# Optimization experiments

Hardware: AMD Instinct MI355X
Metric: run time of the kernel (lower is better)

## Reference

```python
import jax, jax.numpy as jnp
import numpy as np

EPS = 1e-8
TOPK = 10


def setup_inputs() -> dict:
    key = jax.random.key(0)
    kz, ky = jax.random.split(key)
    B, C, T = 128, 512, 512
    Z = jax.random.normal(kz, (B, C, T), dtype=jnp.float32)
    Y = jax.random.normal(ky, (B, C, T), dtype=jnp.float32)
    return {"Z": Z, "Y": Y}


def reference(Z, Y):
    B = Z.shape[0]
    x = Z.reshape(B, -1)  # [B, D]
    y = Y.reshape(B, -1)  # [B, D]
    # cosine similarity: sim[i, j] = x[i] . y[j] / max(|x[i]| * |y[j]|, eps)
    dots = jnp.einsum("id,jd->ij", x, y)  # [B, B]
    xn = jnp.linalg.norm(x, axis=1)  # [B]
    yn = jnp.linalg.norm(y, axis=1)  # [B]
    sim = dots / jnp.maximum(xn[:, None] * yn[None, :], EPS)
    sim = sim.T  # rows now indexed by Y, cols by Z (as in original)
    diags = jnp.arange(B)
    top1accuracy = jnp.mean((jnp.argmax(sim, axis=1) == diags).astype(jnp.float32))
    _, topk_idx = jax.lax.top_k(sim, TOPK)  # [B, 10]
    top10accuracy = jnp.mean(jnp.any(topk_idx == diags[:, None], axis=1).astype(jnp.float32))
    return (top1accuracy, top10accuracy)
```

## Files before the change

kernel.cpp:

```cpp
#include <hip/hip_runtime.h>
#include <hip/hip_bf16.h>
#include <math.h>


#define DIMD 262144

typedef short  bf16x8  __attribute__((ext_vector_type(8)));
typedef float  floatx4 __attribute__((ext_vector_type(4)));

union FragU { uint4 u; bf16x8 v; };

__global__ __launch_bounds__(256, 3)
void mfma_dot_kernel(const float* __restrict__ Z, const float* __restrict__ Y,
                     float* __restrict__ partials, float* __restrict__ norms,
                     int NT) {
    __shared__ __align__(16) ushort planes[4][128][40];
    __shared__ float nrm[256];

    const int tid = threadIdx.x;
    const int lid = tid & 63;
    const int w   = tid >> 6;

    const int srow = tid >> 3;
    const int q    = tid & 7;

    const int m0 = 64 * (w & 1);
    const int n0 = 64 * (w >> 1);
    const int fr = lid & 15;
    const int fk = (lid >> 4) * 8;

    floatx4 acc[4][4];
#pragma unroll
    for (int a = 0; a < 4; ++a)
#pragma unroll
        for (int b = 0; b < 4; ++b)
            acc[a][b] = (floatx4){0.f, 0.f, 0.f, 0.f};

    nrm[tid] = 0.f;

    const size_t kbase = (size_t)blockIdx.x * ((size_t)NT * 32);
    size_t off[4];
#pragma unroll
    for (int i = 0; i < 4; ++i)
        off[i] = (size_t)(32 * i + srow) * DIMD + kbase + 4 * q;

    float4 zr[4], yr[4];
#pragma unroll
    for (int i = 0; i < 4; ++i) zr[i] = *(const float4*)(Z + off[i]);
#pragma unroll
    for (int i = 0; i < 4; ++i) yr[i] = *(const float4*)(Y + off[i]);

#pragma unroll 1
    for (int t = 0; t < NT; ++t) {
        __syncthreads();

#pragma unroll
        for (int i = 0; i < 4; ++i) {
            const float4 v = zr[i];
            const uint h0 = __float_as_uint(v.x) >> 16, h1 = __float_as_uint(v.y) >> 16;
            const uint h2 = __float_as_uint(v.z) >> 16, h3 = __float_as_uint(v.w) >> 16;
            const uint l0 = __float_as_uint(v.x - __uint_as_float(h0 << 16)) >> 16;
            const uint l1 = __float_as_uint(v.y - __uint_as_float(h1 << 16)) >> 16;
            const uint l2 = __float_as_uint(v.z - __uint_as_float(h2 << 16)) >> 16;
            const uint l3 = __float_as_uint(v.w - __uint_as_float(h3 << 16)) >> 16;
            *(uint2*)&planes[0][32 * i + srow][4 * q] =
                make_uint2(h0 | (h1 << 16), h2 | (h3 << 16));
            *(uint2*)&planes[1][32 * i + srow][4 * q] =
                make_uint2(l0 | (l1 << 16), l2 | (l3 << 16));
            const float s = v.x * v.x + v.y * v.y + v.z * v.z + v.w * v.w;
            atomicAdd(&nrm[32 * i + srow], s);
        }
#pragma unroll
        for (int i = 0; i < 4; ++i) {
            const float4 v = yr[i];
            const uint h0 = __float_as_uint(v.x) >> 16, h1 = __float_as_uint(v.y) >> 16;
            const uint h2 = __float_as_uint(v.z) >> 16, h3 = __float_as_uint(v.w) >> 16;
            const uint l0 = __float_as_uint(v.x - __uint_as_float(h0 << 16)) >> 16;
            const uint l1 = __float_as_uint(v.y - __uint_as_float(h1 << 16)) >> 16;
            const uint l2 = __float_as_uint(v.z - __uint_as_float(h2 << 16)) >> 16;
            const uint l3 = __float_as_uint(v.w - __uint_as_float(h3 << 16)) >> 16;
            *(uint2*)&planes[2][32 * i + srow][4 * q] =
                make_uint2(h0 | (h1 << 16), h2 | (h3 << 16));
            *(uint2*)&planes[3][32 * i + srow][4 * q] =
                make_uint2(l0 | (l1 << 16), l2 | (l3 << 16));
            const float s = v.x * v.x + v.y * v.y + v.z * v.z + v.w * v.w;
            atomicAdd(&nrm[128 + 32 * i + srow], s);
        }

        if (t + 1 < NT) {
            const size_t ko = (size_t)(t + 1) * 32;
#pragma unroll
            for (int i = 0; i < 4; ++i) zr[i] = *(const float4*)(Z + off[i] + ko);
#pragma unroll
            for (int i = 0; i < 4; ++i) yr[i] = *(const float4*)(Y + off[i] + ko);
        }

        __syncthreads();

        FragU bh[4], bl[4];
#pragma unroll
        for (int tn = 0; tn < 4; ++tn) {
            bh[tn].u = *(const uint4*)&planes[2][n0 + 16 * tn + fr][fk];
            bl[tn].u = *(const uint4*)&planes[3][n0 + 16 * tn + fr][fk];
        }
#pragma unroll
        for (int tm = 0; tm < 4; ++tm) {
            FragU ah, al;
            ah.u = *(const uint4*)&planes[0][m0 + 16 * tm + fr][fk];
            al.u = *(const uint4*)&planes[1][m0 + 16 * tm + fr][fk];
#pragma unroll
            for (int tn = 0; tn < 4; ++tn) {
                acc[tm][tn] = __builtin_amdgcn_mfma_f32_16x16x32_bf16(ah.v, bh[tn].v, acc[tm][tn], 0, 0, 0);
                acc[tm][tn] = __builtin_amdgcn_mfma_f32_16x16x32_bf16(ah.v, bl[tn].v, acc[tm][tn], 0, 0, 0);
                acc[tm][tn] = __builtin_amdgcn_mfma_f32_16x16x32_bf16(al.v, bh[tn].v, acc[tm][tn], 0, 0, 0);
            }
        }
    }

    __syncthreads();
    atomicAdd(&norms[tid], nrm[tid]);

    float* P = partials + (size_t)blockIdx.x * 16384;
    const int rq = (lid >> 4) * 4;
#pragma unroll
    for (int tm = 0; tm < 4; ++tm)
#pragma unroll
        for (int tn = 0; tn < 4; ++tn)
#pragma unroll
            for (int r = 0; r < 4; ++r)
                P[(size_t)(m0 + 16 * tm + rq + r) * 128 + (n0 + 16 * tn + fr)] =
                    acc[tm][tn][r];
}

#define BK   16
#define LSTR 132
__global__ __launch_bounds__(256)
void dot_norm_atomic(const float* __restrict__ Z, const float* __restrict__ Y,
                     float* __restrict__ dots, float* __restrict__ norms,
                     int KC) {
    __shared__ float lA[BK][LSTR];
    __shared__ float lB[BK][LSTR];
    const int tid = threadIdx.x;
    const int tx = tid & 15, ty = tid >> 4;
    const int r0 = ty * 8, c0 = tx * 8;
    const int rowm = tid >> 2, kq = tid & 3;
    float acc[8][8];
#pragma unroll
    for (int i = 0; i < 8; ++i)
#pragma unroll
        for (int j = 0; j < 8; ++j) acc[i][j] = 0.f;
    float a2s0 = 0.f, a2s1 = 0.f, b2s0 = 0.f, b2s1 = 0.f;
    const size_t kbase = (size_t)blockIdx.x * KC;
    const size_t offA0 = (size_t)rowm * DIMD + kbase + kq * 4;
    const size_t offA1 = (size_t)(rowm + 64) * DIMD + kbase + kq * 4;
    const int niter = KC / BK;
#pragma unroll 1
    for (int t = 0; t < niter; ++t) {
        const size_t ko = (size_t)t * BK;
        const float4 av0 = *(const float4*)(Z + offA0 + ko);
        const float4 av1 = *(const float4*)(Z + offA1 + ko);
        const float4 bv0 = *(const float4*)(Y + offA0 + ko);
        const float4 bv1 = *(const float4*)(Y + offA1 + ko);
        a2s0 += av0.x*av0.x + av0.y*av0.y + av0.z*av0.z + av0.w*av0.w;
        a2s1 += av1.x*av1.x + av1.y*av1.y + av1.z*av1.z + av1.w*av1.w;
        b2s0 += bv0.x*bv0.x + bv0.y*bv0.y + bv0.z*bv0.z + bv0.w*bv0.w;
        b2s1 += bv1.x*bv1.x + bv1.y*bv1.y + bv1.z*bv1.z + bv1.w*bv1.w;
        __syncthreads();
        const int kk = kq * 4;
        lA[kk+0][rowm]    = av0.x; lA[kk+1][rowm]    = av0.y;
        lA[kk+2][rowm]    = av0.z; lA[kk+3][rowm]    = av0.w;
        lA[kk+0][rowm+64] = av1.x; lA[kk+1][rowm+64] = av1.y;
        lA[kk+2][rowm+64] = av1.z; lA[kk+3][rowm+64] = av1.w;
        lB[kk+0][rowm]    = bv0.x; lB[kk+1][rowm]    = bv0.y;
        lB[kk+2][rowm]    = bv0.z; lB[kk+3][rowm]    = bv0.w;
        lB[kk+0][rowm+64] = bv1.x; lB[kk+1][rowm+64] = bv1.y;
        lB[kk+2][rowm+64] = bv1.z; lB[kk+3][rowm+64] = bv1.w;
        __syncthreads();
#pragma unroll
        for (int k = 0; k < BK; ++k) {
            const float4 a0 = *(const float4*)&lA[k][r0];
            const float4 a1 = *(const float4*)&lA[k][r0 + 4];
            const float4 b0 = *(const float4*)&lB[k][c0];
            const float4 b1 = *(const float4*)&lB[k][c0 + 4];
            const float a[8] = {a0.x,a0.y,a0.z,a0.w,a1.x,a1.y,a1.z,a1.w};
            const float b[8] = {b0.x,b0.y,b0.z,b0.w,b1.x,b1.y,b1.z,b1.w};
#pragma unroll
            for (int i = 0; i < 8; ++i)
#pragma unroll
                for (int j = 0; j < 8; ++j)
                    acc[i][j] = fmaf(a[i], b[j], acc[i][j]);
        }
    }
    __syncthreads();
    float* nrm = &lA[0][0];
    nrm[tid] = 0.f;
    __syncthreads();
    atomicAdd(&nrm[rowm],            a2s0);
    atomicAdd(&nrm[rowm + 64],       a2s1);
    atomicAdd(&nrm[128 + rowm],      b2s0);
    atomicAdd(&nrm[128 + rowm + 64], b2s1);
    __syncthreads();
    atomicAdd(&norms[tid], nrm[tid]);
#pragma unroll
    for (int i = 0; i < 8; ++i)
#pragma unroll
        for (int j = 0; j < 8; ++j)
            atomicAdd(&dots[(size_t)(r0 + i) * 128 + (c0 + j)], acc[i][j]);
}

__global__ __launch_bounds__(256)
void reduce_stage1(const float* __restrict__ partials, float* __restrict__ stage,
                   int per_chunk) {
    const int g = blockIdx.x * 256 + threadIdx.x;
    const int f4 = g & 4095;
    const int chunk = g >> 12;
    const float4* p = (const float4*)partials;
    float4 s = make_float4(0.f, 0.f, 0.f, 0.f);
    const size_t base = (size_t)chunk * per_chunk;
    for (int k = 0; k < per_chunk; ++k) {
        const float4 v = p[(base + k) * 4096 + f4];
        s.x += v.x; s.y += v.y; s.z += v.z; s.w += v.w;
    }
    ((float4*)stage)[(size_t)chunk * 4096 + f4] = s;
}

__global__ __launch_bounds__(128)
void rank_kernel(const float* __restrict__ stage, const float* __restrict__ norms,
                 float* __restrict__ out, int nchunks) {
    __shared__ float sim[128];
    __shared__ int cnt;
    const int a = blockIdx.x;
    const int b = threadIdx.x;
    float s = 0.f;
    for (int c = 0; c < nchunks; ++c)
        s += stage[(size_t)c * 16384 + (size_t)b * 128 + a];
    const float v = s / fmaxf(sqrtf(norms[b]) * sqrtf(norms[128 + a]), 1e-8f);
    sim[b] = v;
    if (b == 0) cnt = 0;
    __syncthreads();
    const float diag = sim[a];
    if (b != a && v > diag) atomicAdd(&cnt, 1);
    __syncthreads();
    if (b == 0) {
        if (cnt == 0) atomicAdd(&out[0], 1.0f / 128.0f);
        if (cnt < 10) atomicAdd(&out[1], 1.0f / 128.0f);
    }
}

extern "C" void kernel_launch(void* const* d_in, const int* in_sizes, int n_in,
                              void* d_out, int out_size, void* d_ws, size_t ws_size,
                              hipStream_t stream) {
    const float* Z = (const float*)d_in[0];
    const float* Y = (const float*)d_in[1];
    float* dots     = (float*)d_ws;
    float* norms    = dots + 128 * 128;
    float* stage    = norms + 256;
    float* partials = stage + 32 * 16384;
    float* out      = (float*)d_out;

    const size_t head_floats = 128 * 128 + 256 + 32 * 16384;
    int nb = 0;
    const int cands[3] = {1024, 512, 256};
    for (int c = 0; c < 3; ++c) {
        if ((head_floats + (size_t)cands[c] * 16384) * sizeof(float) <= ws_size) {
            nb = cands[c];
            break;
        }
    }

    hipMemsetAsync(d_ws, 0, (128 * 128 + 256) * sizeof(float), stream);
    hipMemsetAsync(d_out, 0, 2 * sizeof(float), stream);

    if (nb > 0) {
        mfma_dot_kernel<<<nb, 256, 0, stream>>>(Z, Y, partials, norms,
                                                DIMD / nb / 32);
        reduce_stage1<<<512, 256, 0, stream>>>(partials, stage, nb / 32);
        rank_kernel<<<128, 128, 0, stream>>>(stage, norms, out, 32);
    } else {
        dot_norm_atomic<<<512, 256, 0, stream>>>(Z, Y, dots, norms, DIMD / 512);
        rank_kernel<<<128, 128, 0, stream>>>(dots, norms, out, 1);
    }
}
```

Measured before the change: 359.4 us.

## Use 512-thread blocks with register double-buffered loads and shuffle norm reduction

Doubles the block size to 512 threads so each of 8 waves computes a 64x32 output tile, and halves the grid to 512 blocks, which gives fewer partials for the reduce stage. Global loads are double-buffered in registers two K-steps ahead to hide more memory latency. Norms are now kept in per-thread registers and reduced with wave shuffles instead of LDS atomics, and offsets use 32-bit math. The trade is higher register pressure under launch bounds of 512 threads with 4 blocks per SM, plus fewer blocks in flight.

```diff
diff --git a/kernel.cpp b/kernel.cpp
--- a/kernel.cpp
+++ b/kernel.cpp
@@ -10,12 +10,11 @@
 
 union FragU { uint4 u; bf16x8 v; };
 
-__global__ __launch_bounds__(256, 3)
+__global__ __launch_bounds__(512, 4)
 void mfma_dot_kernel(const float* __restrict__ Z, const float* __restrict__ Y,
                      float* __restrict__ partials, float* __restrict__ norms,
                      int NT) {
     __shared__ __align__(16) ushort planes[4][128][40];
-    __shared__ float nrm[256];
 
     const int tid = threadIdx.x;
     const int lid = tid & 63;
@@ -24,82 +23,69 @@
     const int srow = tid >> 3;
     const int q    = tid & 7;
 
-    const int m0 = 64 * (w & 1);
-    const int n0 = 64 * (w >> 1);
+    const int m0 = 64 * (w >> 2);
+    const int n0 = 32 * (w & 3);
     const int fr = lid & 15;
     const int fk = (lid >> 4) * 8;
 
-    floatx4 acc[4][4];
+    floatx4 acc[4][2];
 #pragma unroll
     for (int a = 0; a < 4; ++a)
 #pragma unroll
-        for (int b = 0; b < 4; ++b)
+        for (int b = 0; b < 2; ++b)
             acc[a][b] = (floatx4){0.f, 0.f, 0.f, 0.f};
 
-    nrm[tid] = 0.f;
-
-    const size_t kbase = (size_t)blockIdx.x * ((size_t)NT * 32);
-    size_t off[4];
-#pragma unroll
-    for (int i = 0; i < 4; ++i)
-        off[i] = (size_t)(32 * i + srow) * DIMD + kbase + 4 * q;
-
-    float4 zr[4], yr[4];
-#pragma unroll
-    for (int i = 0; i < 4; ++i) zr[i] = *(const float4*)(Z + off[i]);
-#pragma unroll
-    for (int i = 0; i < 4; ++i) yr[i] = *(const float4*)(Y + off[i]);
-
-#pragma unroll 1
-    for (int t = 0; t < NT; ++t) {
-        __syncthreads();
-
-#pragma unroll
-        for (int i = 0; i < 4; ++i) {
-            const float4 v = zr[i];
-            const uint h0 = __float_as_uint(v.x) >> 16, h1 = __float_as_uint(v.y) >> 16;
-            const uint h2 = __float_as_uint(v.z) >> 16, h3 = __float_as_uint(v.w) >> 16;
-            const uint l0 = __float_as_uint(v.x - __uint_as_float(h0 << 16)) >> 16;
-            const uint l1 = __float_as_uint(v.y - __uint_as_float(h1 << 16)) >> 16;
-            const uint l2 = __float_as_uint(v.z - __uint_as_float(h2 << 16)) >> 16;
-            const uint l3 = __float_as_uint(v.w - __uint_as_float(h3 << 16)) >> 16;
-            *(uint2*)&planes[0][32 * i + srow][4 * q] =
-                make_uint2(h0 | (h1 << 16), h2 | (h3 << 16));
-            *(uint2*)&planes[1][32 * i + srow][4 * q] =
-                make_uint2(l0 | (l1 << 16), l2 | (l3 << 16));
-            const float s = v.x * v.x + v.y * v.y + v.z * v.z + v.w * v.w;
-            atomicAdd(&nrm[32 * i + srow], s);
-        }
-#pragma unroll
-        for (int i = 0; i < 4; ++i) {
-            const float4 v = yr[i];
-            const uint h0 = __float_as_uint(v.x) >> 16, h1 = __float_as_uint(v.y) >> 16;
-            const uint h2 = __float_as_uint(v.z) >> 16, h3 = __float_as_uint(v.w) >> 16;
-            const uint l0 = __float_as_uint(v.x - __uint_as_float(h0 << 16)) >> 16;
-            const uint l1 = __float_as_uint(v.y - __uint_as_float(h1 << 16)) >> 16;
-            const uint l2 = __float_as_uint(v.z - __uint_as_float(h2 << 16)) >> 16;
-            const uint l3 = __float_as_uint(v.w - __uint_as_float(h3 << 16)) >> 16;
-            *(uint2*)&planes[2][32 * i + srow][4 * q] =
-                make_uint2(h0 | (h1 << 16), h2 | (h3 << 16));
-            *(uint2*)&planes[3][32 * i + srow][4 * q] =
-                make_uint2(l0 | (l1 << 16), l2 | (l3 << 16));
-            const float s = v.x * v.x + v.y * v.y + v.z * v.z + v.w * v.w;
-            atomicAdd(&nrm[128 + 32 * i + srow], s);
-        }
-
-        if (t + 1 < NT) {
-            const size_t ko = (size_t)(t + 1) * 32;
-#pragma unroll
-            for (int i = 0; i < 4; ++i) zr[i] = *(const float4*)(Z + off[i] + ko);
-#pragma unroll
-            for (int i = 0; i < 4; ++i) yr[i] = *(const float4*)(Y + off[i] + ko);
-        }
-
-        __syncthreads();
-
-        FragU bh[4], bl[4];
-#pragma unroll
-        for (int tn = 0; tn < 4; ++tn) {
+    float z2[2] = {0.f, 0.f}, y2[2] = {0.f, 0.f};
+
+    const uint kbase = (uint)blockIdx.x * (uint)(NT * 32);
+    const uint off0  = (uint)srow * (uint)DIMD + kbase + 4u * (uint)q;
+    const uint off1  = off0 + 64u * (uint)DIMD;
+
+    float4 za[2], ya[2], zb[2], yb[2];
+    za[0] = *(const float4*)(Z + off0);      za[1] = *(const float4*)(Z + off1);
+    ya[0] = *(const float4*)(Y + off0);      ya[1] = *(const float4*)(Y + off1);
+    zb[0] = *(const float4*)(Z + off0 + 32); zb[1] = *(const float4*)(Z + off1 + 32);
+    yb[0] = *(const float4*)(Y + off0 + 32); yb[1] = *(const float4*)(Y + off1 + 32);
+
+    auto convstore = [&](const float4 (&zr)[2], const float4 (&yr)[2]) {
+#pragma unroll
+        for (int i = 0; i < 2; ++i) {
+            const int row = srow + 64 * i;
+            {
+                const float4 v = zr[i];
+                const uint h0 = __float_as_uint(v.x) >> 16, h1 = __float_as_uint(v.y) >> 16;
+                const uint h2 = __float_as_uint(v.z) >> 16, h3 = __float_as_uint(v.w) >> 16;
+                const uint l0 = __float_as_uint(v.x - __uint_as_float(h0 << 16)) >> 16;
+                const uint l1 = __float_as_uint(v.y - __uint_as_float(h1 << 16)) >> 16;
+                const uint l2 = __float_as_uint(v.z - __uint_as_float(h2 << 16)) >> 16;
+                const uint l3 = __float_as_uint(v.w - __uint_as_float(h3 << 16)) >> 16;
+                *(uint2*)&planes[0][row][4 * q] =
+                    make_uint2(h0 | (h1 << 16), h2 | (h3 << 16));
+                *(uint2*)&planes[1][row][4 * q] =
+                    make_uint2(l0 | (l1 << 16), l2 | (l3 << 16));
+                z2[i] += v.x * v.x + v.y * v.y + v.z * v.z + v.w * v.w;
+            }
+            {
+                const float4 v = yr[i];
+                const uint h0 = __float_as_uint(v.x) >> 16, h1 = __float_as_uint(v.y) >> 16;
+                const uint h2 = __float_as_uint(v.z) >> 16, h3 = __float_as_uint(v.w) >> 16;
+                const uint l0 = __float_as_uint(v.x - __uint_as_float(h0 << 16)) >> 16;
+                const uint l1 = __float_as_uint(v.y - __uint_as_float(h1 << 16)) >> 16;
+                const uint l2 = __float_as_uint(v.z - __uint_as_float(h2 << 16)) >> 16;
+                const uint l3 = __float_as_uint(v.w - __uint_as_float(h3 << 16)) >> 16;
+                *(uint2*)&planes[2][row][4 * q] =
+                    make_uint2(h0 | (h1 << 16), h2 | (h3 << 16));
+                *(uint2*)&planes[3][row][4 * q] =
+                    make_uint2(l0 | (l1 << 16), l2 | (l3 << 16));
+                y2[i] += v.x * v.x + v.y * v.y + v.z * v.z + v.w * v.w;
+            }
+        }
+    };
+
+    auto mfma_phase = [&]() {
+        FragU bh[2], bl[2];
+#pragma unroll
+        for (int tn = 0; tn < 2; ++tn) {
             bh[tn].u = *(const uint4*)&planes[2][n0 + 16 * tn + fr][fk];
             bl[tn].u = *(const uint4*)&planes[3][n0 + 16 * tn + fr][fk];
         }
@@ -109,23 +95,55 @@
             ah.u = *(const uint4*)&planes[0][m0 + 16 * tm + fr][fk];
             al.u = *(const uint4*)&planes[1][m0 + 16 * tm + fr][fk];
 #pragma unroll
-            for (int tn = 0; tn < 4; ++tn) {
+            for (int tn = 0; tn < 2; ++tn) {
                 acc[tm][tn] = __builtin_amdgcn_mfma_f32_16x16x32_bf16(ah.v, bh[tn].v, acc[tm][tn], 0, 0, 0);
                 acc[tm][tn] = __builtin_amdgcn_mfma_f32_16x16x32_bf16(ah.v, bl[tn].v, acc[tm][tn], 0, 0, 0);
                 acc[tm][tn] = __builtin_amdgcn_mfma_f32_16x16x32_bf16(al.v, bh[tn].v, acc[tm][tn], 0, 0, 0);
             }
         }
-    }
-
-    __syncthreads();
-    atomicAdd(&norms[tid], nrm[tid]);
+    };
+
+#pragma unroll 1
+    for (int t = 0; t < NT; t += 2) {
+        __syncthreads();
+        convstore(za, ya);
+        if (t + 2 < NT) {
+            const uint ko = (uint)(t + 2) * 32u;
+            za[0] = *(const float4*)(Z + off0 + ko); za[1] = *(const float4*)(Z + off1 + ko);
+            ya[0] = *(const float4*)(Y + off0 + ko); ya[1] = *(const float4*)(Y + off1 + ko);
+        }
+        __syncthreads();
+        mfma_phase();
+
+        __syncthreads();
+        convstore(zb, yb);
+        if (t + 3 < NT) {
+            const uint ko = (uint)(t + 3) * 32u;
+            zb[0] = *(const float4*)(Z + off0 + ko); zb[1] = *(const float4*)(Z + off1 + ko);
+            yb[0] = *(const float4*)(Y + off0 + ko); yb[1] = *(const float4*)(Y + off1 + ko);
+        }
+        __syncthreads();
+        mfma_phase();
+    }
+
+#pragma unroll
+    for (int m = 1; m <= 4; m <<= 1) {
+        z2[0] += __shfl_xor(z2[0], m); z2[1] += __shfl_xor(z2[1], m);
+        y2[0] += __shfl_xor(y2[0], m); y2[1] += __shfl_xor(y2[1], m);
+    }
+    if (q == 0) {
+        atomicAdd(&norms[srow],            z2[0]);
+        atomicAdd(&norms[srow + 64],       z2[1]);
+        atomicAdd(&norms[128 + srow],      y2[0]);
+        atomicAdd(&norms[128 + srow + 64], y2[1]);
+    }
 
     float* P = partials + (size_t)blockIdx.x * 16384;
     const int rq = (lid >> 4) * 4;
 #pragma unroll
     for (int tm = 0; tm < 4; ++tm)
 #pragma unroll
-        for (int tn = 0; tn < 4; ++tn)
+        for (int tn = 0; tn < 2; ++tn)
 #pragma unroll
             for (int r = 0; r < 4; ++r)
                 P[(size_t)(m0 + 16 * tm + rq + r) * 128 + (n0 + 16 * tn + fr)] =
@@ -260,8 +278,8 @@
 
     const size_t head_floats = 128 * 128 + 256 + 32 * 16384;
     int nb = 0;
-    const int cands[3] = {1024, 512, 256};
-    for (int c = 0; c < 3; ++c) {
+    const int cands[2] = {512, 256};
+    for (int c = 0; c < 2; ++c) {
         if ((head_floats + (size_t)cands[c] * 16384) * sizeof(float) <= ws_size) {
             nb = cands[c];
             break;
@@ -272,7 +290,7 @@
     hipMemsetAsync(d_out, 0, 2 * sizeof(float), stream);
 
     if (nb > 0) {
-        mfma_dot_kernel<<<nb, 256, 0, stream>>>(Z, Y, partials, norms,
+        mfma_dot_kernel<<<nb, 512, 0, stream>>>(Z, Y, partials, norms,
                                                 DIMD / nb / 32);
         reduce_stage1<<<512, 256, 0, stream>>>(partials, stage, nb / 32);
         rank_kernel<<<128, 128, 0, stream>>>(stage, norms, out, 32);
```

Measured after the change: 317.9 us. 11.5% less time.
